# Optimization experiments

Measured on AMD Instinct MI355X. Metric: run time of the kernel, lower is better.

The kernel has to match this reference:

```python
import jax, jax.numpy as jnp
import numpy as np

N, M, D = 4096, 65536, 256

def setup_inputs() -> dict:
    key = jax.random.key(0)
    k1, k2 = jax.random.split(key)
    x = jax.random.normal(k1, (N, D), dtype=jnp.float32)
    target_set = jax.random.normal(k2, (M, D), dtype=jnp.float32)  # [M, D] database
    return {"x": x, "target_set": target_set}

def reference(x, target_set):
    # L2 metric branch of NNDistance.
    # target_set_norm_squared: [1, M] precomputed at init in the original module.
    t_norm_sq = jnp.sum(target_set * target_set, axis=1)[None, :]  # [1, M]
    x_norm_sq = jnp.sum(x * x, axis=1, keepdims=True)              # [N, 1]
    d2 = x_norm_sq + t_norm_sq - 2.0 * jnp.matmul(x, target_set.T)  # [N, M]
    dists = jnp.sqrt(jnp.maximum(d2, 0.0))
    # torch.min(dists, dim=1) returns (values, indices)
    values = jnp.min(dists, axis=1)
    indices = jnp.argmin(dists, axis=1)
    return values, indices
```

## Files before the change

kernel.cpp:

```cpp
#include <hip/hip_runtime.h>
#include <float.h>
#include <math.h>

#define N_ROWS 4096
#define M_TGT  65536
#define DDIM   256

typedef short bf16x8 __attribute__((ext_vector_type(8)));
typedef float f32x4 __attribute__((ext_vector_type(4)));
typedef unsigned short ushort4_t __attribute__((ext_vector_type(4)));

__device__ inline unsigned short f2bf(float f) {
  union { float f; unsigned u; } c; c.f = f;
  unsigned u = c.u;
  unsigned r = (u + 0x7FFFu + ((u >> 16) & 1u)) >> 16;
  return (unsigned short)r;
}

__device__ inline void gload_lds16(const void* g, void* l) {
  __builtin_amdgcn_global_load_lds(
      (const __attribute__((address_space(1))) void*)g,
      (__attribute__((address_space(3))) void*)l, 16, 0, 0);
}

#define MFMA16(a, b, c) __builtin_amdgcn_mfma_f32_16x16x32_bf16(a, b, c, 0, 0, 0)

__global__ __launch_bounds__(256) void conv_norm_all(
    const float* __restrict__ x, const float* __restrict__ t,
    unsigned short* __restrict__ xb, unsigned short* __restrict__ tb,
    float* __restrict__ xn, float* __restrict__ tn) {
  int wave = threadIdx.x >> 6;
  int lane = threadIdx.x & 63;
  int row  = blockIdx.x * 4 + wave;
  const float* src;
  unsigned short* db;
  float* dn;
  if (row < N_ROWS) {
    src = x + (size_t)row * DDIM;
    db  = xb + (size_t)row * DDIM;
    dn  = xn + row;
  } else {
    int r = row - N_ROWS;
    if (r >= M_TGT) return;
    src = t + (size_t)r * DDIM;
    db  = tb + (size_t)r * DDIM;
    dn  = tn + r;
  }
  float4 v = *(const float4*)(src + lane * 4);
  float ss = v.x * v.x + v.y * v.y + v.z * v.z + v.w * v.w;
  ushort4_t o;
  o[0] = f2bf(v.x); o[1] = f2bf(v.y); o[2] = f2bf(v.z); o[3] = f2bf(v.w);
  *(ushort4_t*)(db + lane * 4) = o;
  #pragma unroll
  for (int off = 32; off > 0; off >>= 1) ss += __shfl_xor(ss, off, 64);
  if (lane == 0) *dn = ss;
}

#define GBM 128
#define GBN2 256
#define GBK 64
#define NCB 512
#define NGRP 2048
#define MARGIN 1.5f

__global__ __launch_bounds__(512) void nn_gemm_bf16(
    const unsigned short* __restrict__ xb, const unsigned short* __restrict__ tb,
    const float* __restrict__ tn, float* __restrict__ bmv32) {
  __shared__ __align__(16) unsigned short sX[GBM * GBK];
  __shared__ __align__(16) unsigned short sT[GBN2 * GBK];
  __shared__ float smin[8][128];

  const int tid  = threadIdx.x;
  const int lane = tid & 63;
  const int wid  = tid >> 6;
  const int wt   = wid >> 1;
  const int wx   = wid & 1;
  const int ln   = lane & 15;
  const int cg   = lane >> 4;

  const int bid = blockIdx.x;
  const int xcd = bid & 7;
  const int w   = bid >> 3;
  const int rb  = w & 31;
  const int cb  = xcd * 32 + (w >> 5);
  const int row0 = rb * GBM;
  const int col0 = cb * GBN2;

  int rqa[2], sqa[2];
  #pragma unroll
  for (int i = 0; i < 2; ++i) {
    int q = i * 512 + tid;
    rqa[i] = q >> 3;
    sqa[i] = (q & 7) ^ (rqa[i] & 7);
  }
  int rqb[4], sqb[4];
  #pragma unroll
  for (int i = 0; i < 4; ++i) {
    int q = i * 512 + tid;
    rqb[i] = q >> 3;
    sqb[i] = (q & 7) ^ (rqb[i] & 7);
  }
  char* sXc = (char*)sX;
  char* sTc = (char*)sT;

  f32x4 acc[4][4];
  const f32x4 zero = {0.0f, 0.0f, 0.0f, 0.0f};
  #pragma unroll
  for (int m = 0; m < 4; ++m)
    #pragma unroll
    for (int n = 0; n < 4; ++n) acc[m][n] = zero;

  #pragma unroll
  for (int kc = 0; kc < DDIM; kc += GBK) {
    __syncthreads();
    #pragma unroll
    for (int i = 0; i < 2; ++i)
      gload_lds16(xb + (size_t)(row0 + rqa[i]) * DDIM + kc + sqa[i] * 8,
                  sXc + (i * 512 + tid) * 16);
    #pragma unroll
    for (int i = 0; i < 4; ++i)
      gload_lds16(tb + (size_t)(col0 + rqb[i]) * DDIM + kc + sqb[i] * 8,
                  sTc + (i * 512 + tid) * 16);
    __syncthreads();

    bf16x8 tf[4][2], xf[4][2];
    #pragma unroll
    for (int m = 0; m < 4; ++m) {
      int r = wt * 64 + m * 16 + ln;
      #pragma unroll
      for (int kk = 0; kk < 2; ++kk) {
        int p = (kk * 4 + cg) ^ (r & 7);
        tf[m][kk] = *(const bf16x8*)(sTc + r * 128 + p * 16);
      }
    }
    #pragma unroll
    for (int n = 0; n < 4; ++n) {
      int r = wx * 64 + n * 16 + ln;
      #pragma unroll
      for (int kk = 0; kk < 2; ++kk) {
        int p = (kk * 4 + cg) ^ (r & 7);
        xf[n][kk] = *(const bf16x8*)(sXc + r * 128 + p * 16);
      }
    }
    #pragma unroll
    for (int kk = 0; kk < 2; ++kk)
      #pragma unroll
      for (int m = 0; m < 4; ++m)
        #pragma unroll
        for (int n = 0; n < 4; ++n)
          acc[m][n] = MFMA16(tf[m][kk], xf[n][kk], acc[m][n]);
  }

  float tnc[4][4];
  #pragma unroll
  for (int m = 0; m < 4; ++m)
    #pragma unroll
    for (int j = 0; j < 4; ++j)
      tnc[m][j] = tn[col0 + wt * 64 + m * 16 + cg * 4 + j];

  float vres[2][4];
  #pragma unroll
  for (int mh2 = 0; mh2 < 2; ++mh2) {
    #pragma unroll
    for (int n = 0; n < 4; ++n) {
      float v = FLT_MAX;
      #pragma unroll
      for (int mi = 0; mi < 2; ++mi) {
        int m = mh2 * 2 + mi;
        #pragma unroll
        for (int j = 0; j < 4; ++j)
          v = fminf(v, fmaf(-2.0f, acc[m][n][j], tnc[m][j]));
      }
      v = fminf(v, __shfl_xor(v, 16, 64));
      v = fminf(v, __shfl_xor(v, 32, 64));
      vres[mh2][n] = v;
    }
  }

  if (cg == 0) {
    #pragma unroll
    for (int mh2 = 0; mh2 < 2; ++mh2)
      #pragma unroll
      for (int n = 0; n < 4; ++n)
        smin[wt * 2 + mh2][wx * 64 + n * 16 + ln] = vres[mh2][n];
  }
  __syncthreads();
  if (tid < 128) {
    float4 o0, o1;
    o0.x = smin[0][tid]; o0.y = smin[1][tid];
    o0.z = smin[2][tid]; o0.w = smin[3][tid];
    o1.x = smin[4][tid]; o1.y = smin[5][tid];
    o1.z = smin[6][tid]; o1.w = smin[7][tid];
    float* dst = &bmv32[(size_t)(row0 + tid) * NGRP + (size_t)cb * 8];
    *(float4*)dst = o0;
    *(float4*)(dst + 4) = o1;
  }
}

__global__ __launch_bounds__(256) void nn_exact_fine(
    const float* __restrict__ x, const float* __restrict__ t,
    const float* __restrict__ xn, const float* __restrict__ tn,
    const float* __restrict__ bmv32, float* __restrict__ out) {
  __shared__ float wmin[4];
  __shared__ int   clist[NGRP];
  __shared__ int   cnt;
  __shared__ float rv[256];
  __shared__ int   ri[256];

  const int row = blockIdx.x;
  const int tid = threadIdx.x;
  const float* brow = bmv32 + (size_t)row * NGRP;

  if (tid == 0) cnt = 0;
  float4 v0 = *(const float4*)(brow + tid * 8);
  float4 v1 = *(const float4*)(brow + tid * 8 + 4);
  float lmin = fminf(fminf(fminf(v0.x, v0.y), fminf(v0.z, v0.w)),
                     fminf(fminf(v1.x, v1.y), fminf(v1.z, v1.w)));
  #pragma unroll
  for (int off = 32; off > 0; off >>= 1)
    lmin = fminf(lmin, __shfl_xor(lmin, off, 64));
  if ((tid & 63) == 0) wmin[tid >> 6] = lmin;
  __syncthreads();
  const float thr =
      fminf(fminf(wmin[0], wmin[1]), fminf(wmin[2], wmin[3])) + MARGIN;

  {
    float vv[8] = {v0.x, v0.y, v0.z, v0.w, v1.x, v1.y, v1.z, v1.w};
    #pragma unroll
    for (int k = 0; k < 8; ++k) {
      if (vv[k] <= thr) {
        int p = atomicAdd(&cnt, 1);
        clist[p] = tid * 8 + k;
      }
    }
  }
  __syncthreads();
  const int nc = cnt;

  float best = FLT_MAX;
  int   bidx = 0x7FFFFFFF;
  const float xnr = xn[row];
  const float* xrow = x + (size_t)row * DDIM;

  for (int ci = 0; ci < nc; ci += 8) {
    int slot = ci + (tid >> 5);
    if (slot < nc) {
      int col = clist[slot] * 32 + (tid & 31);
      const float* trow = t + (size_t)col * DDIM;
      float acc = 0.0f;
      for (int kq = 0; kq < DDIM; kq += 4) {
        float4 xv = *(const float4*)(xrow + kq);
        float4 tv = *(const float4*)(trow + kq);
        acc = fmaf(xv.x, tv.x, acc);
        acc = fmaf(xv.y, tv.y, acc);
        acc = fmaf(xv.z, tv.z, acc);
        acc = fmaf(xv.w, tv.w, acc);
      }
      float d2 = xnr + tn[col] - 2.0f * acc;
      if (d2 < best || (d2 == best && col < bidx)) { best = d2; bidx = col; }
    }
  }
  rv[tid] = best; ri[tid] = bidx;
  __syncthreads();
  for (int s = 128; s >= 1; s >>= 1) {
    if (tid < s) {
      float vo = rv[tid + s]; int io = ri[tid + s];
      if (vo < rv[tid] || (vo == rv[tid] && io < ri[tid])) { rv[tid] = vo; ri[tid] = io; }
    }
    __syncthreads();
  }
  if (tid == 0) {
    out[row] = sqrtf(fmaxf(rv[0], 0.0f));
    out[N_ROWS + row] = (float)ri[0];
  }
}

#define MGBM 128
#define MGBN 128

__global__ __launch_bounds__(256) void nn_gemm_mid(
    const unsigned short* __restrict__ xb, const unsigned short* __restrict__ tb,
    const float* __restrict__ tn, float* __restrict__ bmv) {
  __shared__ __align__(16) unsigned short sX[MGBM * GBK];
  __shared__ __align__(16) unsigned short sT[MGBN * GBK];
  __shared__ float smin[2][128];

  const int tid  = threadIdx.x;
  const int lane = tid & 63;
  const int wid  = tid >> 6;
  const int wt   = wid >> 1;
  const int wx   = wid & 1;
  const int ln   = lane & 15;
  const int cg   = lane >> 4;

  const int bid = blockIdx.x;
  const int xcd = bid & 7;
  const int wgi = bid >> 3;
  const int rb  = wgi & 31;
  const int cb  = xcd * 64 + (wgi >> 5);
  const int row0 = rb * MGBM;
  const int col0 = cb * MGBN;

  int rq[4], sq[4];
  #pragma unroll
  for (int i = 0; i < 4; ++i) {
    int q = i * 256 + tid;
    rq[i] = q >> 3;
    sq[i] = (q & 7) ^ (rq[i] & 7);
  }
  char* sXc = (char*)sX;
  char* sTc = (char*)sT;

  f32x4 acc[4][4];
  const f32x4 zero = {0.0f, 0.0f, 0.0f, 0.0f};
  #pragma unroll
  for (int m = 0; m < 4; ++m)
    #pragma unroll
    for (int n = 0; n < 4; ++n) acc[m][n] = zero;

  #pragma unroll
  for (int kc = 0; kc < DDIM; kc += GBK) {
    __syncthreads();
    #pragma unroll
    for (int i = 0; i < 4; ++i)
      gload_lds16(xb + (size_t)(row0 + rq[i]) * DDIM + kc + sq[i] * 8,
                  sXc + i * 4096 + wid * 1024);
    #pragma unroll
    for (int i = 0; i < 4; ++i)
      gload_lds16(tb + (size_t)(col0 + rq[i]) * DDIM + kc + sq[i] * 8,
                  sTc + i * 4096 + wid * 1024);
    __syncthreads();

    bf16x8 tf[4][2], xf[4][2];
    #pragma unroll
    for (int m = 0; m < 4; ++m) {
      int r = wt * 64 + m * 16 + ln;
      #pragma unroll
      for (int kk = 0; kk < 2; ++kk) {
        int p = (kk * 4 + cg) ^ (r & 7);
        tf[m][kk] = *(const bf16x8*)(sTc + r * 128 + p * 16);
      }
    }
    #pragma unroll
    for (int n = 0; n < 4; ++n) {
      int r = wx * 64 + n * 16 + ln;
      #pragma unroll
      for (int kk = 0; kk < 2; ++kk) {
        int p = (kk * 4 + cg) ^ (r & 7);
        xf[n][kk] = *(const bf16x8*)(sXc + r * 128 + p * 16);
      }
    }
    #pragma unroll
    for (int kk = 0; kk < 2; ++kk)
      #pragma unroll
      for (int m = 0; m < 4; ++m)
        #pragma unroll
        for (int n = 0; n < 4; ++n)
          acc[m][n] = MFMA16(tf[m][kk], xf[n][kk], acc[m][n]);
  }

  float tnc[4][4];
  #pragma unroll
  for (int m = 0; m < 4; ++m)
    #pragma unroll
    for (int j = 0; j < 4; ++j)
      tnc[m][j] = tn[col0 + wt * 64 + m * 16 + cg * 4 + j];

  float res[4];
  #pragma unroll
  for (int n = 0; n < 4; ++n) {
    float v = FLT_MAX;
    #pragma unroll
    for (int m = 0; m < 4; ++m)
      #pragma unroll
      for (int j = 0; j < 4; ++j)
        v = fminf(v, fmaf(-2.0f, acc[m][n][j], tnc[m][j]));
    v = fminf(v, __shfl_xor(v, 16, 64));
    v = fminf(v, __shfl_xor(v, 32, 64));
    res[n] = v;
  }

  __syncthreads();
  if (cg == 0) {
    #pragma unroll
    for (int n = 0; n < 4; ++n)
      smin[wt][wx * 64 + n * 16 + ln] = res[n];
  }
  __syncthreads();
  if (tid < 128)
    bmv[(size_t)(row0 + tid) * NCB + cb] = fminf(smin[0][tid], smin[1][tid]);
}

__global__ __launch_bounds__(256) void nn_exact_mid(
    const float* __restrict__ x, const float* __restrict__ t,
    const float* __restrict__ xn, const float* __restrict__ tn,
    const float* __restrict__ bmv, float* __restrict__ out) {
  __shared__ float sv[NCB];
  __shared__ int   clist[NCB];
  __shared__ int   cnt;
  __shared__ float wmin[4];
  __shared__ float rv[256];
  __shared__ int   ri[256];

  const int row = blockIdx.x;
  const int tid = threadIdx.x;

  if (tid == 0) cnt = 0;
  float lmin = FLT_MAX;
  #pragma unroll
  for (int e = tid; e < NCB; e += 256) {
    float v = bmv[(size_t)row * NCB + e];
    sv[e] = v;
    lmin = fminf(lmin, v);
  }
  #pragma unroll
  for (int off = 32; off > 0; off >>= 1) lmin = fminf(lmin, __shfl_xor(lmin, off, 64));
  if ((tid & 63) == 0) wmin[tid >> 6] = lmin;
  __syncthreads();
  const float g = fminf(fminf(wmin[0], wmin[1]), fminf(wmin[2], wmin[3]));

  #pragma unroll
  for (int e = tid; e < NCB; e += 256) {
    if (sv[e] <= g + MARGIN) {
      int p = atomicAdd(&cnt, 1);
      clist[p] = e;
    }
  }
  __syncthreads();
  const int nc = cnt;

  float best = FLT_MAX;
  int   bidx = 0x7FFFFFFF;
  const float xnr = xn[row];
  const float* xrow = x + (size_t)row * DDIM;

  for (int ci = 0; ci < nc; ci += 2) {
    int slot = ci + (tid >> 7);
    if (slot < nc) {
      int col = clist[slot] * 128 + (tid & 127);
      const float* trow = t + (size_t)col * DDIM;
      float acc = 0.0f;
      for (int kq = 0; kq < DDIM; kq += 4) {
        float4 xv = *(const float4*)(xrow + kq);
        float4 tv = *(const float4*)(trow + kq);
        acc = fmaf(xv.x, tv.x, acc);
        acc = fmaf(xv.y, tv.y, acc);
        acc = fmaf(xv.z, tv.z, acc);
        acc = fmaf(xv.w, tv.w, acc);
      }
      float d2 = xnr + tn[col] - 2.0f * acc;
      if (d2 < best || (d2 == best && col < bidx)) { best = d2; bidx = col; }
    }
  }
  rv[tid] = best; ri[tid] = bidx;
  __syncthreads();
  for (int s = 128; s >= 1; s >>= 1) {
    if (tid < s) {
      float vo = rv[tid + s]; int io = ri[tid + s];
      if (vo < rv[tid] || (vo == rv[tid] && io < ri[tid])) { rv[tid] = vo; ri[tid] = io; }
    }
    __syncthreads();
  }
  if (tid == 0) {
    out[row] = sqrtf(fmaxf(rv[0], 0.0f));
    out[N_ROWS + row] = (float)ri[0];
  }
}

#define BM 64
#define BN 64
#define KC 16
#define S_STRIPS 32
#define PADM 68

__global__ __launch_bounds__(256) void norms_kernel_fb(
    const float* __restrict__ x, const float* __restrict__ t,
    float* __restrict__ xn, float* __restrict__ tn) {
  int wave = threadIdx.x >> 6;
  int lane = threadIdx.x & 63;
  int row  = blockIdx.x * 4 + wave;
  const float* src; float* dst;
  if (row < N_ROWS) { src = x + (size_t)row * DDIM; dst = xn + row; }
  else {
    int r = row - N_ROWS;
    if (r >= M_TGT) return;
    src = t + (size_t)r * DDIM; dst = tn + r;
  }
  float4 v = *(const float4*)(src + lane * 4);
  float s = v.x * v.x + v.y * v.y + v.z * v.z + v.w * v.w;
  #pragma unroll
  for (int off = 32; off > 0; off >>= 1) s += __shfl_xor(s, off, 64);
  if (lane == 0) *dst = s;
}

__global__ __launch_bounds__(256) void nn_main_fb(
    const float* __restrict__ x, const float* __restrict__ t,
    const float* __restrict__ xn, const float* __restrict__ tn,
    float* __restrict__ pmin, int* __restrict__ pidx) {
  __shared__ float sx[KC][PADM];
  __shared__ float st[KC][PADM];
  const int tid = threadIdx.x;
  const int rb = blockIdx.x;
  const int strip = blockIdx.y;
  const int tx = tid & 15, ty = tid >> 4;
  const int row0 = rb * BM;
  const int col_start = strip * (M_TGT / S_STRIPS);
  const int ntiles = (M_TGT / S_STRIPS) / BN;
  const int srow = tid >> 2;
  const int kq = (tid & 3) * 4;

  float runMin[4]; int runIdx[4];
  #pragma unroll
  for (int r = 0; r < 4; ++r) { runMin[r] = FLT_MAX; runIdx[r] = 0; }
  float xnr[4];
  #pragma unroll
  for (int r = 0; r < 4; ++r) xnr[r] = xn[row0 + ty * 4 + r];

  for (int tile = 0; tile < ntiles; ++tile) {
    const int cbk = col_start + tile * BN;
    float acc[4][4];
    #pragma unroll
    for (int r = 0; r < 4; ++r)
      #pragma unroll
      for (int c = 0; c < 4; ++c) acc[r][c] = 0.0f;
    #pragma unroll 1
    for (int kc = 0; kc < DDIM; kc += KC) {
      float4 xv = *(const float4*)(x + (size_t)(row0 + srow) * DDIM + kc + kq);
      float4 tv = *(const float4*)(t + (size_t)(cbk + srow) * DDIM + kc + kq);
      __syncthreads();
      sx[kq + 0][srow] = xv.x; sx[kq + 1][srow] = xv.y;
      sx[kq + 2][srow] = xv.z; sx[kq + 3][srow] = xv.w;
      st[kq + 0][srow] = tv.x; st[kq + 1][srow] = tv.y;
      st[kq + 2][srow] = tv.z; st[kq + 3][srow] = tv.w;
      __syncthreads();
      #pragma unroll
      for (int k = 0; k < KC; ++k) {
        float4 xa = *(const float4*)&sx[k][ty * 4];
        float4 tb2 = *(const float4*)&st[k][tx * 4];
        float xr[4] = {xa.x, xa.y, xa.z, xa.w};
        float tc[4] = {tb2.x, tb2.y, tb2.z, tb2.w};
        #pragma unroll
        for (int r = 0; r < 4; ++r)
          #pragma unroll
          for (int c = 0; c < 4; ++c)
            acc[r][c] = fmaf(xr[r], tc[c], acc[r][c]);
      }
    }
    #pragma unroll
    for (int r = 0; r < 4; ++r)
      #pragma unroll
      for (int c = 0; c < 4; ++c) {
        int col = cbk + tx * 4 + c;
        float d2 = xnr[r] + tn[col] - 2.0f * acc[r][c];
        if (d2 < runMin[r]) { runMin[r] = d2; runIdx[r] = col; }
      }
  }
  __syncthreads();
  float* redv = &sx[0][0];
  int*   redi = (int*)&st[0][0];
  #pragma unroll
  for (int r = 0; r < 4; ++r) {
    int lrow = ty * 4 + r;
    redv[lrow * 16 + tx] = runMin[r];
    redi[lrow * 16 + tx] = runIdx[r];
  }
  __syncthreads();
  if (tid < 64) {
    float best = FLT_MAX; int bi = 0;
    #pragma unroll
    for (int j = 0; j < 16; ++j) {
      float v = redv[tid * 16 + j];
      int   i = redi[tid * 16 + j];
      if (v < best || (v == best && i < bi)) { best = v; bi = i; }
    }
    int grow = row0 + tid;
    pmin[(size_t)grow * S_STRIPS + strip] = best;
    pidx[(size_t)grow * S_STRIPS + strip] = bi;
  }
}

__global__ __launch_bounds__(256) void reduce_final_fb(
    const float* __restrict__ pmin, const int* __restrict__ pidx,
    float* __restrict__ out) {
  int row = blockIdx.x * 256 + threadIdx.x;
  if (row >= N_ROWS) return;
  float best = FLT_MAX; int bi = 0;
  #pragma unroll 4
  for (int s = 0; s < S_STRIPS; ++s) {
    float v = pmin[(size_t)row * S_STRIPS + s];
    int   i = pidx[(size_t)row * S_STRIPS + s];
    if (v < best || (v == best && i < bi)) { best = v; bi = i; }
  }
  out[row] = sqrtf(fmaxf(best, 0.0f));
  out[N_ROWS + row] = (float)bi;
}

extern "C" void kernel_launch(void* const* d_in, const int* in_sizes, int n_in,
                              void* d_out, int out_size, void* d_ws, size_t ws_size,
                              hipStream_t stream) {
  const float* x = (const float*)d_in[0];
  const float* t = (const float*)d_in[1];
  float* ws = (float*)d_ws;
  float* out = (float*)d_out;

  float* xn = ws;
  float* tn = ws + N_ROWS;

  const size_t f_bmvF = (size_t)N_ROWS + M_TGT;
  const size_t f_xbF  = f_bmvF + (size_t)N_ROWS * NGRP;
  const size_t f_tbF  = f_xbF + ((size_t)N_ROWS * DDIM) / 2;
  const size_t need_fine = (f_tbF + ((size_t)M_TGT * DDIM) / 2) * sizeof(float);

  const size_t f_bmvM = (size_t)N_ROWS + M_TGT;
  const size_t f_xbM  = f_bmvM + (size_t)N_ROWS * NCB;
  const size_t f_tbM  = f_xbM + ((size_t)N_ROWS * DDIM) / 2;
  const size_t need_mid = (f_tbM + ((size_t)M_TGT * DDIM) / 2) * sizeof(float);

  if (ws_size >= need_fine) {
    float* bmv32 = ws + f_bmvF;
    unsigned short* xb = (unsigned short*)(ws + f_xbF);
    unsigned short* tb = (unsigned short*)(ws + f_tbF);

    conv_norm_all<<<(N_ROWS + M_TGT) / 4, 256, 0, stream>>>(x, t, xb, tb, xn, tn);
    nn_gemm_bf16<<<(N_ROWS / GBM) * (M_TGT / GBN2), 512, 0, stream>>>(xb, tb, tn, bmv32);
    nn_exact_fine<<<N_ROWS, 256, 0, stream>>>(x, t, xn, tn, bmv32, out);
  } else if (ws_size >= need_mid) {
    float* bmv = ws + f_bmvM;
    unsigned short* xb = (unsigned short*)(ws + f_xbM);
    unsigned short* tb = (unsigned short*)(ws + f_tbM);

    conv_norm_all<<<(N_ROWS + M_TGT) / 4, 256, 0, stream>>>(x, t, xb, tb, xn, tn);
    nn_gemm_mid<<<(N_ROWS / MGBM) * NCB, 256, 0, stream>>>(xb, tb, tn, bmv);
    nn_exact_mid<<<N_ROWS, 256, 0, stream>>>(x, t, xn, tn, bmv, out);
  } else {
    norms_kernel_fb<<<(N_ROWS + M_TGT) / 4, 256, 0, stream>>>(x, t, xn, tn);
    float* pmin = ws + N_ROWS + M_TGT;
    int*   pidx = (int*)(ws + N_ROWS + M_TGT + (size_t)N_ROWS * S_STRIPS);
    dim3 grid(N_ROWS / BM, S_STRIPS);
    nn_main_fb<<<grid, 256, 0, stream>>>(x, t, xn, tn, pmin, pidx);
    reduce_final_fb<<<(N_ROWS + 255) / 256, 256, 0, stream>>>(pmin, pidx, out);
  }
}
```

Before: 190.7 us.

## Double-buffer LDS tiles with K=32 chunks in bf16 GEMM kernel

Restructures the main bf16 GEMM's K loop from four 64-wide chunks, each fully loaded and then synced, into eight 32-wide chunks held in double-buffered LDS. The next chunk is prefetched while MFMAs run on the current one, and the LDS swizzle is adjusted for 64-byte rows. It also raises wave priority around the MFMA block. This is meant to hide global-to-LDS latency, at the cost of more barriers and smaller MFMA batches per sync.

```diff
diff --git a/kernel.cpp b/kernel.cpp
--- a/kernel.cpp
+++ b/kernel.cpp
@@ -58,7 +58,6 @@
 
 #define GBM 128
 #define GBN2 256
-#define GBK 64
 #define NCB 512
 #define NGRP 2048
 #define MARGIN 1.5f
@@ -66,8 +65,8 @@
 __global__ __launch_bounds__(512) void nn_gemm_bf16(
     const unsigned short* __restrict__ xb, const unsigned short* __restrict__ tb,
     const float* __restrict__ tn, float* __restrict__ bmv32) {
-  __shared__ __align__(16) unsigned short sX[GBM * GBK];
-  __shared__ __align__(16) unsigned short sT[GBN2 * GBK];
+  __shared__ __align__(16) unsigned short sXb[2][GBM * 32];
+  __shared__ __align__(16) unsigned short sTb[2][GBN2 * 32];
   __shared__ float smin[8][128];
 
   const int tid  = threadIdx.x;
@@ -86,22 +85,20 @@
   const int row0 = rb * GBM;
   const int col0 = cb * GBN2;
 
-  int rqa[2], sqa[2];
+  const int rXq = tid >> 2;
+  const int sXo = ((tid & 3) ^ ((rXq >> 1) & 3)) * 8;
+  int rTq[2], sTo[2];
   #pragma unroll
   for (int i = 0; i < 2; ++i) {
     int q = i * 512 + tid;
-    rqa[i] = q >> 3;
-    sqa[i] = (q & 7) ^ (rqa[i] & 7);
-  }
-  int rqb[4], sqb[4];
-  #pragma unroll
-  for (int i = 0; i < 4; ++i) {
-    int q = i * 512 + tid;
-    rqb[i] = q >> 3;
-    sqb[i] = (q & 7) ^ (rqb[i] & 7);
-  }
-  char* sXc = (char*)sX;
-  char* sTc = (char*)sT;
+    rTq[i] = q >> 2;
+    sTo[i] = ((q & 3) ^ ((rTq[i] >> 1) & 3)) * 8;
+  }
+  char* sXc = (char*)&sXb[0][0];
+  char* sTc = (char*)&sTb[0][0];
+  const unsigned short* gX = xb + (size_t)(row0 + rXq) * DDIM + sXo;
+  const unsigned short* gT0 = tb + (size_t)(col0 + rTq[0]) * DDIM + sTo[0];
+  const unsigned short* gT1 = tb + (size_t)(col0 + rTq[1]) * DDIM + sTo[1];
 
   f32x4 acc[4][4];
   const f32x4 zero = {0.0f, 0.0f, 0.0f, 0.0f};
@@ -110,45 +107,41 @@
     #pragma unroll
     for (int n = 0; n < 4; ++n) acc[m][n] = zero;
 
-  #pragma unroll
-  for (int kc = 0; kc < DDIM; kc += GBK) {
-    __syncthreads();
-    #pragma unroll
-    for (int i = 0; i < 2; ++i)
-      gload_lds16(xb + (size_t)(row0 + rqa[i]) * DDIM + kc + sqa[i] * 8,
-                  sXc + (i * 512 + tid) * 16);
-    #pragma unroll
-    for (int i = 0; i < 4; ++i)
-      gload_lds16(tb + (size_t)(col0 + rqb[i]) * DDIM + kc + sqb[i] * 8,
-                  sTc + (i * 512 + tid) * 16);
-    __syncthreads();
-
-    bf16x8 tf[4][2], xf[4][2];
+  gload_lds16(gX, sXc + tid * 16);
+  gload_lds16(gT0, sTc + tid * 16);
+  gload_lds16(gT1, sTc + 8192 + tid * 16);
+  __syncthreads();
+
+  #pragma unroll
+  for (int t = 0; t < 8; ++t) {
+    const int bufc = t & 1;
+    if (t < 7) {
+      const int bufn = bufc ^ 1;
+      gload_lds16(gX + (t + 1) * 32, sXc + bufn * 8192 + tid * 16);
+      gload_lds16(gT0 + (t + 1) * 32, sTc + bufn * 16384 + tid * 16);
+      gload_lds16(gT1 + (t + 1) * 32, sTc + bufn * 16384 + 8192 + tid * 16);
+    }
+    bf16x8 tf[4], xf[4];
     #pragma unroll
     for (int m = 0; m < 4; ++m) {
       int r = wt * 64 + m * 16 + ln;
-      #pragma unroll
-      for (int kk = 0; kk < 2; ++kk) {
-        int p = (kk * 4 + cg) ^ (r & 7);
-        tf[m][kk] = *(const bf16x8*)(sTc + r * 128 + p * 16);
-      }
+      int p = cg ^ ((r >> 1) & 3);
+      tf[m] = *(const bf16x8*)(sTc + bufc * 16384 + r * 64 + p * 16);
     }
     #pragma unroll
     for (int n = 0; n < 4; ++n) {
       int r = wx * 64 + n * 16 + ln;
-      #pragma unroll
-      for (int kk = 0; kk < 2; ++kk) {
-        int p = (kk * 4 + cg) ^ (r & 7);
-        xf[n][kk] = *(const bf16x8*)(sXc + r * 128 + p * 16);
-      }
-    }
-    #pragma unroll
-    for (int kk = 0; kk < 2; ++kk)
-      #pragma unroll
-      for (int m = 0; m < 4; ++m)
-        #pragma unroll
-        for (int n = 0; n < 4; ++n)
-          acc[m][n] = MFMA16(tf[m][kk], xf[n][kk], acc[m][n]);
+      int p = cg ^ ((r >> 1) & 3);
+      xf[n] = *(const bf16x8*)(sXc + bufc * 8192 + r * 64 + p * 16);
+    }
+    __builtin_amdgcn_s_setprio(1);
+    #pragma unroll
+    for (int m = 0; m < 4; ++m)
+      #pragma unroll
+      for (int n = 0; n < 4; ++n)
+        acc[m][n] = MFMA16(tf[m], xf[n], acc[m][n]);
+    __builtin_amdgcn_s_setprio(0);
+    __syncthreads();
   }
 
   float tnc[4][4];
@@ -277,6 +270,7 @@
 
 #define MGBM 128
 #define MGBN 128
+#define GBK 64
 
 __global__ __launch_bounds__(256) void nn_gemm_mid(
     const unsigned short* __restrict__ xb, const unsigned short* __restrict__ tb,
```

Result: slower. 205.9 us (+7.9%).
